# Optimization experiments

Hardware: AMD Instinct MI355X
Metric: run time of the kernel (lower is better)

Reference implementation:

```python
import jax, jax.numpy as jnp
import numpy as np

B, S, D_IN, D_OUT, L = 16, 1024, 768, 768, 2
ALPHA = 0.2  # LeakyReLU negative slope
NEG_INF = -1e12


def setup_inputs() -> dict:
    key = jax.random.key(0)
    ks = jax.random.split(key, 6)
    input_feature = jax.random.normal(ks[0], (B, S, D_IN), dtype=jnp.float32)
    matrix = jax.random.randint(ks[1], (B, S, S), 0, 2, dtype=jnp.int32)
    # per-layer params (stacked along leading L axis)
    sw = 1.0 / np.sqrt(D_IN)
    W = jax.random.uniform(ks[2], (L, D_OUT, D_IN), jnp.float32, -sw, sw)
    Wb = jax.random.uniform(ks[3], (L, D_OUT), jnp.float32, -sw, sw)
    sa = 1.0 / np.sqrt(2 * D_OUT)
    A = jax.random.uniform(ks[4], (L, 2 * D_OUT), jnp.float32, -sa, sa)
    Ab = jax.random.uniform(ks[5], (L,), jnp.float32, -sa, sa)
    return {"input_feature": input_feature, "matrix": matrix,
            "W": W, "Wb": Wb, "A": A, "Ab": Ab}


def reference(input_feature, matrix, W, Wb, A, Ab):
    # Eval mode: dropout(p=0.1, training=False) is identity.
    hidden = input_feature
    mask = matrix > 0  # [B,S,S]
    outs = []
    for l in range(L):
        h = jnp.einsum('bsd,od->bso', hidden, W[l]) + Wb[l]  # [B,S,Dout]
        # a([h_i, h_j]) == h_i @ a_src + h_j @ a_dst + b  (exact separation)
        a_src, a_dst = A[l, :D_OUT], A[l, D_OUT:]
        s_i = h @ a_src  # [B,S]
        s_j = h @ a_dst  # [B,S]
        e = jax.nn.leaky_relu(s_i[:, :, None] + s_j[:, None, :] + Ab[l], ALPHA)
        e = jnp.where(mask, e, NEG_INF)
        attn = jax.nn.softmax(e, axis=1)  # original softmaxes over dim=1
        hidden = jnp.einsum('bij,bjd->bid', attn, h)
        outs.append(hidden)
    return jnp.stack(outs)  # [L,B,S,Dout]
```

## Files before the change

kernel.cpp:

```cpp
#include <hip/hip_runtime.h>
#include <cstddef>

#define SS 1024
#define DF 768
#define NBATCH 16
#define GAT_ALPHA 0.2f

typedef _Float16 f16x8 __attribute__((ext_vector_type(8)));
typedef _Float16 f16x4 __attribute__((ext_vector_type(4)));
typedef float f32x4 __attribute__((ext_vector_type(4)));

__device__ __forceinline__ void gload16(const void* g, void* l) {
  __builtin_amdgcn_global_load_lds(
      (const __attribute__((address_space(1))) void*)g,
      (__attribute__((address_space(3))) void*)l, 16, 0, 0);
}

__device__ __forceinline__ float lrelu(float t) {
  return fmaxf(t, GAT_ALPHA * t);
}

__global__ __launch_bounds__(256) void f32tof16_k(const float* __restrict__ in,
                                                  _Float16* __restrict__ out,
                                                  int n) {
  int idx = (blockIdx.x * 256 + threadIdx.x) * 4;
  if (idx + 3 < n) {
    float4 v = *(const float4*)&in[idx];
    f16x4 o;
    o[0] = (_Float16)v.x;
    o[1] = (_Float16)v.y;
    o[2] = (_Float16)v.z;
    o[3] = (_Float16)v.w;
    *(f16x4*)&out[idx] = o;
  }
}

__global__ __launch_bounds__(256) void pack_k(const int* __restrict__ mask,
                                              unsigned char* __restrict__ bm) {
  const size_t t = (size_t)blockIdx.x * 256 + threadIdx.x;
  const int* mp = mask + t * 8;
  const int4 a = *(const int4*)mp;
  const int4 c = *(const int4*)(mp + 4);
  unsigned v = (unsigned)(a.x > 0) | ((unsigned)(a.y > 0) << 1) |
               ((unsigned)(a.z > 0) << 2) | ((unsigned)(a.w > 0) << 3) |
               ((unsigned)(c.x > 0) << 4) | ((unsigned)(c.y > 0) << 5) |
               ((unsigned)(c.z > 0) << 6) | ((unsigned)(c.w > 0) << 7);
  bm[t] = (unsigned char)v;
}


__global__ __launch_bounds__(512, 2) void gemm1_k(
    const _Float16* __restrict__ X16, const _Float16* __restrict__ W16,
    const float* __restrict__ Wbl, _Float16* __restrict__ hT16) {
  __shared__ __align__(16) char smem[131072];
  const int flat = blockIdx.x;
  const int swz = (flat & 7) * 32 + (flat >> 3);
  const int m0 = (swz >> 1) * 128;
  const int n0 = (swz & 1) * 384;
  const int tid = threadIdx.x;
  const int w = tid >> 6, lane = tid & 63;

  const int srow = w * 16 + (lane >> 2);
  const int sk8 = ((lane & 3) ^ ((lane >> 3) & 3)) * 8;
  const int rby = ((lane >> 4) ^ ((lane >> 1) & 3)) * 16;
  const int rrow = lane & 15;

  f32x4 acc[8][3];
#pragma unroll
  for (int mi = 0; mi < 8; ++mi)
#pragma unroll
    for (int ni = 0; ni < 3; ++ni) acc[mi][ni] = (f32x4)(0.f);

#define STGA1(s, kt)                                                       \
  gload16(&X16[(size_t)(m0 + srow) * DF + (kt) * 32 + sk8],                \
          smem + (s) * 32768 + w * 1024)
#define STGB1(s, kt, q)                                                    \
  gload16(&W16[(size_t)(n0 + (q) * 128 + srow) * DF + (kt) * 32 + sk8],    \
          smem + (s) * 32768 + 8192 + (q) * 8192 + w * 1024)

  const int NT = DF / 32;
  STGA1(0, 0); STGB1(0, 0, 0); STGB1(0, 0, 1); STGB1(0, 0, 2);
  STGA1(1, 1); STGB1(1, 1, 0); STGB1(1, 1, 1); STGB1(1, 1, 2);
  asm volatile("s_waitcnt vmcnt(4)" ::: "memory");
  asm volatile("s_barrier" ::: "memory");

  for (int t = 0; t < NT; ++t) {
    const int s = t & 3;
    const char* Ab = smem + s * 32768;
    const char* Bb = smem + s * 32768 + 8192;
    f16x8 bfr[3], afr[4];
#pragma unroll
    for (int ni = 0; ni < 3; ++ni)
      bfr[ni] = *(const f16x8*)(Bb + (w * 48 + ni * 16 + rrow) * 64 + rby);
#pragma unroll
    for (int mi = 0; mi < 4; ++mi)
      afr[mi] = *(const f16x8*)(Ab + (mi * 16 + rrow) * 64 + rby);
    if (t + 2 < NT) {
      STGA1((t + 2) & 3, t + 2);
      STGB1((t + 2) & 3, t + 2, 0);
    }
    asm volatile("s_barrier" ::: "memory");
    __builtin_amdgcn_s_setprio(1);
#pragma unroll
    for (int mi = 0; mi < 4; ++mi)
#pragma unroll
      for (int ni = 0; ni < 3; ++ni)
        acc[mi][ni] = __builtin_amdgcn_mfma_f32_16x16x32_f16(
            afr[mi], bfr[ni], acc[mi][ni], 0, 0, 0);
    __builtin_amdgcn_s_setprio(0);
    asm volatile("s_barrier" ::: "memory");
#pragma unroll
    for (int mi = 0; mi < 4; ++mi)
      afr[mi] = *(const f16x8*)(Ab + ((mi + 4) * 16 + rrow) * 64 + rby);
    if (t + 2 < NT) {
      STGB1((t + 2) & 3, t + 2, 1);
      STGB1((t + 2) & 3, t + 2, 2);
    }
    if (t < NT - 2)
      asm volatile("s_waitcnt vmcnt(4)" ::: "memory");
    else
      asm volatile("s_waitcnt vmcnt(0)" ::: "memory");
    asm volatile("s_barrier" ::: "memory");
    __builtin_amdgcn_s_setprio(1);
#pragma unroll
    for (int mi = 0; mi < 4; ++mi)
#pragma unroll
      for (int ni = 0; ni < 3; ++ni)
        acc[mi + 4][ni] = __builtin_amdgcn_mfma_f32_16x16x32_f16(
            afr[mi], bfr[ni], acc[mi + 4][ni], 0, 0, 0);
    __builtin_amdgcn_s_setprio(0);
    asm volatile("s_barrier" ::: "memory");
  }
#undef STGA1
#undef STGB1

  _Float16* tb = (_Float16*)smem + (size_t)w * 6528;
  const int cg = lane >> 4, cr = lane & 15;
  float bias[3];
#pragma unroll
  for (int ni = 0; ni < 3; ++ni) bias[ni] = Wbl[n0 + w * 48 + ni * 16 + cr];
#pragma unroll
  for (int mi = 0; mi < 8; ++mi) {
#pragma unroll
    for (int ni = 0; ni < 3; ++ni) {
      f16x4 tv;
#pragma unroll
      for (int r = 0; r < 4; ++r)
        tv[r] = (_Float16)(acc[mi][ni][r] + bias[ni]);
      *(f16x4*)&tb[(ni * 16 + cr) * 136 + mi * 16 + cg * 4] = tv;
    }
  }
  const int bb = m0 >> 10, s0 = m0 & 1023;
#pragma unroll
  for (int pass = 0; pass < 12; ++pass) {
    const int c = pass * 4 + (lane >> 4);
    f16x8 v = *(const f16x8*)&tb[c * 136 + (lane & 15) * 8];
    *(f16x8*)&hT16[((size_t)bb * DF + n0 + w * 48 + c) * SS + s0 +
                   (lane & 15) * 8] = v;
  }
}

__global__ __launch_bounds__(512, 2) void gemm2_k(
    const _Float16* __restrict__ P16, const _Float16* __restrict__ hT16,
    float* __restrict__ outl, _Float16* __restrict__ X16n, int writeX) {
  __shared__ __align__(16) char smem[131072];
  const int flat = blockIdx.x;
  const int swz = (flat & 7) * 32 + (flat >> 3);
  const int b = swz >> 4;
  const int i0 = ((swz >> 1) & 7) * 128;
  const int d0 = (swz & 1) * 384;
  const int tid = threadIdx.x;
  const int w = tid >> 6, lane = tid & 63;

  const int srow = w * 16 + (lane >> 2);
  const int sk8 = ((lane & 3) ^ ((lane >> 3) & 3)) * 8;
  const int rby = ((lane >> 4) ^ ((lane >> 1) & 3)) * 16;
  const int rrow = lane & 15;

  const _Float16* Pb = P16 + ((size_t)b << 20);
  const _Float16* hTb = hT16 + (size_t)b * DF * SS;

  f32x4 acc[8][3];
#pragma unroll
  for (int mi = 0; mi < 8; ++mi)
#pragma unroll
    for (int ni = 0; ni < 3; ++ni) acc[mi][ni] = (f32x4)(0.f);

#define STGA2(s, kt)                                                       \
  gload16(&Pb[((size_t)(i0 + srow) << 10) + (kt) * 32 + sk8],              \
          smem + (s) * 32768 + w * 1024)
#define STGB2(s, kt, q)                                                    \
  gload16(&hTb[((size_t)(d0 + (q) * 128 + srow)) * SS + (kt) * 32 + sk8],  \
          smem + (s) * 32768 + 8192 + (q) * 8192 + w * 1024)

  const int NT = SS / 32;
  STGA2(0, 0); STGB2(0, 0, 0); STGB2(0, 0, 1); STGB2(0, 0, 2);
  STGA2(1, 1); STGB2(1, 1, 0); STGB2(1, 1, 1); STGB2(1, 1, 2);
  asm volatile("s_waitcnt vmcnt(4)" ::: "memory");
  asm volatile("s_barrier" ::: "memory");

  for (int t = 0; t < NT; ++t) {
    const int s = t & 3;
    const char* Ab = smem + s * 32768;
    const char* Bb = smem + s * 32768 + 8192;
    f16x8 bfr[3], afr[4];
#pragma unroll
    for (int ni = 0; ni < 3; ++ni)
      bfr[ni] = *(const f16x8*)(Bb + (w * 48 + ni * 16 + rrow) * 64 + rby);
#pragma unroll
    for (int mi = 0; mi < 4; ++mi)
      afr[mi] = *(const f16x8*)(Ab + (mi * 16 + rrow) * 64 + rby);
    if (t + 2 < NT) {
      STGA2((t + 2) & 3, t + 2);
      STGB2((t + 2) & 3, t + 2, 0);
    }
    asm volatile("s_barrier" ::: "memory");
    __builtin_amdgcn_s_setprio(1);
#pragma unroll
    for (int mi = 0; mi < 4; ++mi)
#pragma unroll
      for (int ni = 0; ni < 3; ++ni)
        acc[mi][ni] = __builtin_amdgcn_mfma_f32_16x16x32_f16(
            afr[mi], bfr[ni], acc[mi][ni], 0, 0, 0);
    __builtin_amdgcn_s_setprio(0);
    asm volatile("s_barrier" ::: "memory");
#pragma unroll
    for (int mi = 0; mi < 4; ++mi)
      afr[mi] = *(const f16x8*)(Ab + ((mi + 4) * 16 + rrow) * 64 + rby);
    if (t + 2 < NT) {
      STGB2((t + 2) & 3, t + 2, 1);
      STGB2((t + 2) & 3, t + 2, 2);
    }
    if (t < NT - 2)
      asm volatile("s_waitcnt vmcnt(4)" ::: "memory");
    else
      asm volatile("s_waitcnt vmcnt(0)" ::: "memory");
    asm volatile("s_barrier" ::: "memory");
    __builtin_amdgcn_s_setprio(1);
#pragma unroll
    for (int mi = 0; mi < 4; ++mi)
#pragma unroll
      for (int ni = 0; ni < 3; ++ni)
        acc[mi + 4][ni] = __builtin_amdgcn_mfma_f32_16x16x32_f16(
            afr[mi], bfr[ni], acc[mi + 4][ni], 0, 0, 0);
    __builtin_amdgcn_s_setprio(0);
    asm volatile("s_barrier" ::: "memory");
  }
#undef STGA2
#undef STGB2

  const int cg = lane >> 4, cr = lane & 15;
#pragma unroll
  for (int mi = 0; mi < 8; ++mi) {
#pragma unroll
    for (int ni = 0; ni < 3; ++ni) {
      const int d = d0 + w * 48 + ni * 16 + cr;
      const int row0 = i0 + mi * 16 + cg * 4;
#pragma unroll
      for (int r = 0; r < 4; ++r) {
        float v = acc[mi][ni][r];
        size_t o = ((size_t)b * SS + row0 + r) * DF + d;
        outl[o] = v;
        if (writeX) X16n[o] = (_Float16)v;
      }
    }
  }
}

__global__ __launch_bounds__(256) void rowdots2_k(
    const _Float16* __restrict__ hT, const float* __restrict__ Al,
    float* __restrict__ psi, float* __restrict__ psj) {
  const int dc = blockIdx.x;
  const int b = blockIdx.y;
  const int t = threadIdx.x;
  const int s4 = t * 4;
  __shared__ float sa[48], sd[48];
  if (t < 48) {
    sa[t] = Al[dc * 48 + t];
    sd[t] = Al[DF + dc * 48 + t];
  }
  __syncthreads();
  float as[4] = {0.f, 0.f, 0.f, 0.f}, ad[4] = {0.f, 0.f, 0.f, 0.f};
  const _Float16* hp = hT + ((size_t)b * DF + dc * 48) * SS + s4;
#pragma unroll 4
  for (int q = 0; q < 48; ++q) {
    const f16x4 hv = *(const f16x4*)(hp + (size_t)q * SS);
    const float ws = sa[q], wd = sd[q];
#pragma unroll
    for (int r = 0; r < 4; ++r) {
      const float hf = (float)hv[r];
      as[r] = fmaf(hf, ws, as[r]);
      ad[r] = fmaf(hf, wd, ad[r]);
    }
  }
  const size_t o = (size_t)dc * 16384 + (b << 10) + s4;
  *(float4*)&psi[o] = *(float4*)as;
  *(float4*)&psj[o] = *(float4*)ad;
}

__global__ __launch_bounds__(256) void rowfin_k(const float* __restrict__ psi,
                                                const float* __restrict__ psj,
                                                const float* __restrict__ Abp,
                                                float* __restrict__ si,
                                                float* __restrict__ sjc,
                                                float* __restrict__ refj) {
  const int b = blockIdx.x;
  const int t = threadIdx.x;
  __shared__ float red[256];
  float siv[4], sjv[4];
  float mloc = -1e30f;
#pragma unroll
  for (int q = 0; q < 4; ++q) {
    const int idx = (b << 10) + t + (q << 8);
    float a = 0.f, d = 0.f;
#pragma unroll
    for (int c = 0; c < 16; ++c) {
      a += psi[(size_t)c * 16384 + idx];
      d += psj[(size_t)c * 16384 + idx];
    }
    siv[q] = a;
    sjv[q] = d;
    si[idx] = a;
    mloc = fmaxf(mloc, a);
  }
  red[t] = mloc;
  __syncthreads();
  for (int off = 128; off > 0; off >>= 1) {
    if (t < off) red[t] = fmaxf(red[t], red[t + off]);
    __syncthreads();
  }
  const float maxsi = red[0];
  const float ab = Abp[0];
#pragma unroll
  for (int q = 0; q < 4; ++q) {
    const int idx = (b << 10) + t + (q << 8);
    const float c = sjv[q] + ab;
    sjc[idx] = c;
    refj[idx] = lrelu(maxsi + c);
  }
}

__global__ __launch_bounds__(256) void colsum_k(
    const unsigned char* __restrict__ bm, const float* __restrict__ si,
    const float* __restrict__ sjc, const float* __restrict__ refj,
    float* __restrict__ pden) {
  const int g = blockIdx.x;
  const int b = blockIdx.y;
  const int t = threadIdx.x;
  const int jb = t & 127;
  const int half = t >> 7;
  const int row0 = (g << 5) + (half << 4);
  __shared__ float s_si[32];
  if (t < 32) s_si[t] = si[(b << 10) + (g << 5) + t];
  __syncthreads();
  float sc[8], rf[8];
  *(float4*)&sc[0] = *(const float4*)&sjc[(b << 10) + jb * 8];
  *(float4*)&sc[4] = *(const float4*)&sjc[(b << 10) + jb * 8 + 4];
  *(float4*)&rf[0] = *(const float4*)&refj[(b << 10) + jb * 8];
  *(float4*)&rf[4] = *(const float4*)&refj[(b << 10) + jb * 8 + 4];
  float den[8] = {0.f, 0.f, 0.f, 0.f, 0.f, 0.f, 0.f, 0.f};
  const unsigned char* bp = bm + ((size_t)b << 17) + ((size_t)row0 << 7) + jb;
#pragma unroll 4
  for (int r = 0; r < 16; ++r) {
    const unsigned m = bp[(size_t)r << 7];
    const float siv = s_si[(half << 4) + r];
#pragma unroll
    for (int k = 0; k < 8; ++k) {
      if ((m >> k) & 1) den[k] += __expf(lrelu(siv + sc[k]) - rf[k]);
    }
  }
  const size_t o = ((size_t)(g * 2 + half)) * 16384 + (b << 10) + jb * 8;
  *(float4*)&pden[o] = *(float4*)&den[0];
  *(float4*)&pden[o + 4] = *(float4*)&den[4];
}

__global__ __launch_bounds__(256) void colcomb_k(const float* __restrict__ pden,
                                                 float* __restrict__ rden) {
  const int idx = blockIdx.x * 256 + threadIdx.x;
  float s = 0.f;
#pragma unroll
  for (int c = 0; c < 64; ++c) s += pden[(size_t)c * 16384 + idx];
  rden[idx] = (s > 0.f) ? 1.f / s : -1.f;
}

__global__ __launch_bounds__(256) void punorm2_k(
    const unsigned char* __restrict__ bm, const float* __restrict__ si,
    const float* __restrict__ sjc, const float* __restrict__ refj,
    const float* __restrict__ rden, _Float16* __restrict__ P16) {
  const int g = blockIdx.x;
  const int b = blockIdx.y;
  const int t = threadIdx.x;
  const int jb = t & 127;
  const int half = t >> 7;
  const int row0 = (g << 5) + (half << 4);
  __shared__ float s_si[32];
  if (t < 32) s_si[t] = si[(b << 10) + (g << 5) + t];
  __syncthreads();
  float sc[8], rf[8], rd[8];
  *(float4*)&sc[0] = *(const float4*)&sjc[(b << 10) + jb * 8];
  *(float4*)&sc[4] = *(const float4*)&sjc[(b << 10) + jb * 8 + 4];
  *(float4*)&rf[0] = *(const float4*)&refj[(b << 10) + jb * 8];
  *(float4*)&rf[4] = *(const float4*)&refj[(b << 10) + jb * 8 + 4];
  *(float4*)&rd[0] = *(const float4*)&rden[(b << 10) + jb * 8];
  *(float4*)&rd[4] = *(const float4*)&rden[(b << 10) + jb * 8 + 4];
  const unsigned char* bp = bm + ((size_t)b << 17) + ((size_t)row0 << 7) + jb;
  _Float16* pp = P16 + ((size_t)b << 20) + ((size_t)row0 << 10) + jb * 8;
#pragma unroll 4
  for (int r = 0; r < 16; ++r) {
    const unsigned m = bp[(size_t)r << 7];
    const float siv = s_si[(half << 4) + r];
    f16x8 ph;
#pragma unroll
    for (int k = 0; k < 8; ++k) {
      float p;
      if (rd[k] < 0.f)
        p = 0.0009765625f;
      else if ((m >> k) & 1)
        p = __expf(lrelu(siv + sc[k]) - rf[k]) * rd[k];
      else
        p = 0.f;
      ph[k] = (_Float16)p;
    }
    *(f16x8*)(pp + ((size_t)r << 10)) = ph;
  }
}

extern "C" void kernel_launch(void* const* d_in, const int* in_sizes, int n_in,
                              void* d_out, int out_size, void* d_ws,
                              size_t ws_size, hipStream_t stream) {
  const float* X0 = (const float*)d_in[0];
  const int* mask = (const int*)d_in[1];
  const float* W = (const float*)d_in[2];
  const float* Wb = (const float*)d_in[3];
  const float* A = (const float*)d_in[4];
  const float* Ab = (const float*)d_in[5];
  float* out = (float*)d_out;

  const size_t BSD = (size_t)NBATCH * SS * DF;
  const size_t BSS = (size_t)NBATCH * SS * SS;
  const size_t BS = (size_t)NBATCH * SS;

  char* p = (char*)d_ws;
  _Float16* X16 = (_Float16*)p;   p += BSD * 2;
  _Float16* hT16 = (_Float16*)p;  p += BSD * 2;
  _Float16* P16 = (_Float16*)p;   p += BSS * 2;
  _Float16* W16 = (_Float16*)p;   p += (size_t)2 * DF * DF * 2;
  unsigned char* bmk = (unsigned char*)p; p += BSS / 8;
  float* psi = (float*)p;  p += 16 * BS * 4;
  float* psj = (float*)p;  p += 16 * BS * 4;
  float* pden = (float*)p; p += 64 * BS * 4;
  float* si = (float*)p;   p += BS * 4;
  float* sjc = (float*)p;  p += BS * 4;
  float* refj = (float*)p; p += BS * 4;
  float* rden = (float*)p; p += BS * 4;

  f32tof16_k<<<12288, 256, 0, stream>>>(X0, X16, (int)BSD);
  f32tof16_k<<<1152, 256, 0, stream>>>(W, W16, 2 * DF * DF);
  pack_k<<<8192, 256, 0, stream>>>(mask, bmk);

  for (int l = 0; l < 2; ++l) {
    gemm1_k<<<256, 512, 0, stream>>>(X16, W16 + (size_t)l * DF * DF,
                                     Wb + (size_t)l * DF, hT16);
    rowdots2_k<<<dim3(16, 16), 256, 0, stream>>>(hT16, A + (size_t)l * 2 * DF,
                                                 psi, psj);
    rowfin_k<<<16, 256, 0, stream>>>(psi, psj, Ab + l, si, sjc, refj);
    colsum_k<<<dim3(32, 16), 256, 0, stream>>>(bmk, si, sjc, refj, pden);
    colcomb_k<<<64, 256, 0, stream>>>(pden, rden);
    punorm2_k<<<dim3(32, 16), 256, 0, stream>>>(bmk, si, sjc, refj, rden, P16);
    gemm2_k<<<256, 512, 0, stream>>>(P16, hT16, out + (size_t)l * BSD, X16,
                                     (l == 0) ? 1 : 0);
  }
}
```

Baseline: 268.1 us.

## Fuse attention row-dot products into gemm1 epilogue and simplify GEMM main loop

Computes the per-row a_src/a_dst dot products inside the gemm1 epilogue from the fp16 tile already staged in shared memory. This removes the separate rowdots2 kernel, its re-read of hT16 and its 16-way partial buffers; rowfin now sums only two partials. Both GEMM main loops also load all 8 A fragments at once and issue all four prefetches together, dropping two barriers per iteration. The cost is higher register pressure and extra epilogue synchronisation.

```diff
diff --git a/kernel.cpp b/kernel.cpp
--- a/kernel.cpp
+++ b/kernel.cpp
@@ -51,7 +51,9 @@
 
 __global__ __launch_bounds__(512, 2) void gemm1_k(
     const _Float16* __restrict__ X16, const _Float16* __restrict__ W16,
-    const float* __restrict__ Wbl, _Float16* __restrict__ hT16) {
+    const float* __restrict__ Wbl, const float* __restrict__ Al,
+    _Float16* __restrict__ hT16, float* __restrict__ psi2,
+    float* __restrict__ psj2) {
   __shared__ __align__(16) char smem[131072];
   const int flat = blockIdx.x;
   const int swz = (flat & 7) * 32 + (flat >> 3);
@@ -88,33 +90,19 @@
     const int s = t & 3;
     const char* Ab = smem + s * 32768;
     const char* Bb = smem + s * 32768 + 8192;
-    f16x8 bfr[3], afr[4];
+    f16x8 bfr[3], afr[8];
 #pragma unroll
     for (int ni = 0; ni < 3; ++ni)
       bfr[ni] = *(const f16x8*)(Bb + (w * 48 + ni * 16 + rrow) * 64 + rby);
 #pragma unroll
-    for (int mi = 0; mi < 4; ++mi)
+    for (int mi = 0; mi < 8; ++mi)
       afr[mi] = *(const f16x8*)(Ab + (mi * 16 + rrow) * 64 + rby);
     if (t + 2 < NT) {
-      STGA1((t + 2) & 3, t + 2);
-      STGB1((t + 2) & 3, t + 2, 0);
-    }
-    asm volatile("s_barrier" ::: "memory");
-    __builtin_amdgcn_s_setprio(1);
-#pragma unroll
-    for (int mi = 0; mi < 4; ++mi)
-#pragma unroll
-      for (int ni = 0; ni < 3; ++ni)
-        acc[mi][ni] = __builtin_amdgcn_mfma_f32_16x16x32_f16(
-            afr[mi], bfr[ni], acc[mi][ni], 0, 0, 0);
-    __builtin_amdgcn_s_setprio(0);
-    asm volatile("s_barrier" ::: "memory");
-#pragma unroll
-    for (int mi = 0; mi < 4; ++mi)
-      afr[mi] = *(const f16x8*)(Ab + ((mi + 4) * 16 + rrow) * 64 + rby);
-    if (t + 2 < NT) {
-      STGB1((t + 2) & 3, t + 2, 1);
-      STGB1((t + 2) & 3, t + 2, 2);
+      const int s2 = (t + 2) & 3;
+      STGA1(s2, t + 2);
+      STGB1(s2, t + 2, 0);
+      STGB1(s2, t + 2, 1);
+      STGB1(s2, t + 2, 2);
     }
     if (t < NT - 2)
       asm volatile("s_waitcnt vmcnt(4)" ::: "memory");
@@ -123,18 +111,28 @@
     asm volatile("s_barrier" ::: "memory");
     __builtin_amdgcn_s_setprio(1);
 #pragma unroll
-    for (int mi = 0; mi < 4; ++mi)
+    for (int mi = 0; mi < 8; ++mi)
 #pragma unroll
       for (int ni = 0; ni < 3; ++ni)
-        acc[mi + 4][ni] = __builtin_amdgcn_mfma_f32_16x16x32_f16(
-            afr[mi], bfr[ni], acc[mi + 4][ni], 0, 0, 0);
+        acc[mi][ni] = __builtin_amdgcn_mfma_f32_16x16x32_f16(
+            afr[mi], bfr[ni], acc[mi][ni], 0, 0, 0);
     __builtin_amdgcn_s_setprio(0);
-    asm volatile("s_barrier" ::: "memory");
   }
 #undef STGA1
 #undef STGB1
 
+  __syncthreads();
+
   _Float16* tb = (_Float16*)smem + (size_t)w * 6528;
+  float* asrc = (float*)(smem + 104448);
+  float* adst = asrc + 384;
+  float* pwsi = adst + 384;
+  float* pwsj = pwsi + 1024;
+
+  for (int i = tid; i < 384; i += 512) {
+    asrc[i] = Al[n0 + i];
+    adst[i] = Al[DF + n0 + i];
+  }
   const int cg = lane >> 4, cr = lane & 15;
   float bias[3];
 #pragma unroll
@@ -150,6 +148,36 @@
       *(f16x4*)&tb[(ni * 16 + cr) * 136 + mi * 16 + cg * 4] = tv;
     }
   }
+  __syncthreads();
+
+  const float* wa = asrc + w * 48;
+  const float* wdp = adst + w * 48;
+#pragma unroll
+  for (int rr = 0; rr < 2; ++rr) {
+    const int r = lane + rr * 64;
+    float ps = 0.f, pd = 0.f;
+#pragma unroll 8
+    for (int c = 0; c < 48; ++c) {
+      const float hv = (float)tb[c * 136 + r];
+      ps = fmaf(hv, wa[c], ps);
+      pd = fmaf(hv, wdp[c], pd);
+    }
+    pwsi[w * 128 + r] = ps;
+    pwsj[w * 128 + r] = pd;
+  }
+  __syncthreads();
+  if (tid < 128) {
+    float s = 0.f, d2 = 0.f;
+#pragma unroll
+    for (int ww = 0; ww < 8; ++ww) {
+      s += pwsi[ww * 128 + tid];
+      d2 += pwsj[ww * 128 + tid];
+    }
+    const int nt = swz & 1;
+    psi2[nt * 16384 + m0 + tid] = s;
+    psj2[nt * 16384 + m0 + tid] = d2;
+  }
+
   const int bb = m0 >> 10, s0 = m0 & 1023;
 #pragma unroll
   for (int pass = 0; pass < 12; ++pass) {
@@ -203,33 +231,19 @@
     const int s = t & 3;
     const char* Ab = smem + s * 32768;
     const char* Bb = smem + s * 32768 + 8192;
-    f16x8 bfr[3], afr[4];
+    f16x8 bfr[3], afr[8];
 #pragma unroll
     for (int ni = 0; ni < 3; ++ni)
       bfr[ni] = *(const f16x8*)(Bb + (w * 48 + ni * 16 + rrow) * 64 + rby);
 #pragma unroll
-    for (int mi = 0; mi < 4; ++mi)
+    for (int mi = 0; mi < 8; ++mi)
       afr[mi] = *(const f16x8*)(Ab + (mi * 16 + rrow) * 64 + rby);
     if (t + 2 < NT) {
-      STGA2((t + 2) & 3, t + 2);
-      STGB2((t + 2) & 3, t + 2, 0);
-    }
-    asm volatile("s_barrier" ::: "memory");
-    __builtin_amdgcn_s_setprio(1);
-#pragma unroll
-    for (int mi = 0; mi < 4; ++mi)
-#pragma unroll
-      for (int ni = 0; ni < 3; ++ni)
-        acc[mi][ni] = __builtin_amdgcn_mfma_f32_16x16x32_f16(
-            afr[mi], bfr[ni], acc[mi][ni], 0, 0, 0);
-    __builtin_amdgcn_s_setprio(0);
-    asm volatile("s_barrier" ::: "memory");
-#pragma unroll
-    for (int mi = 0; mi < 4; ++mi)
-      afr[mi] = *(const f16x8*)(Ab + ((mi + 4) * 16 + rrow) * 64 + rby);
-    if (t + 2 < NT) {
-      STGB2((t + 2) & 3, t + 2, 1);
-      STGB2((t + 2) & 3, t + 2, 2);
+      const int s2 = (t + 2) & 3;
+      STGA2(s2, t + 2);
+      STGB2(s2, t + 2, 0);
+      STGB2(s2, t + 2, 1);
+      STGB2(s2, t + 2, 2);
     }
     if (t < NT - 2)
       asm volatile("s_waitcnt vmcnt(4)" ::: "memory");
@@ -238,13 +252,12 @@
     asm volatile("s_barrier" ::: "memory");
     __builtin_amdgcn_s_setprio(1);
 #pragma unroll
-    for (int mi = 0; mi < 4; ++mi)
+    for (int mi = 0; mi < 8; ++mi)
 #pragma unroll
       for (int ni = 0; ni < 3; ++ni)
-        acc[mi + 4][ni] = __builtin_amdgcn_mfma_f32_16x16x32_f16(
-            afr[mi], bfr[ni], acc[mi + 4][ni], 0, 0, 0);
+        acc[mi][ni] = __builtin_amdgcn_mfma_f32_16x16x32_f16(
+            afr[mi], bfr[ni], acc[mi][ni], 0, 0, 0);
     __builtin_amdgcn_s_setprio(0);
-    asm volatile("s_barrier" ::: "memory");
   }
 #undef STGA2
 #undef STGB2
@@ -267,39 +280,8 @@
   }
 }
 
-__global__ __launch_bounds__(256) void rowdots2_k(
-    const _Float16* __restrict__ hT, const float* __restrict__ Al,
-    float* __restrict__ psi, float* __restrict__ psj) {
-  const int dc = blockIdx.x;
-  const int b = blockIdx.y;
-  const int t = threadIdx.x;
-  const int s4 = t * 4;
-  __shared__ float sa[48], sd[48];
-  if (t < 48) {
-    sa[t] = Al[dc * 48 + t];
-    sd[t] = Al[DF + dc * 48 + t];
-  }
-  __syncthreads();
-  float as[4] = {0.f, 0.f, 0.f, 0.f}, ad[4] = {0.f, 0.f, 0.f, 0.f};
-  const _Float16* hp = hT + ((size_t)b * DF + dc * 48) * SS + s4;
-#pragma unroll 4
-  for (int q = 0; q < 48; ++q) {
-    const f16x4 hv = *(const f16x4*)(hp + (size_t)q * SS);
-    const float ws = sa[q], wd = sd[q];
-#pragma unroll
-    for (int r = 0; r < 4; ++r) {
-      const float hf = (float)hv[r];
-      as[r] = fmaf(hf, ws, as[r]);
-      ad[r] = fmaf(hf, wd, ad[r]);
-    }
-  }
-  const size_t o = (size_t)dc * 16384 + (b << 10) + s4;
-  *(float4*)&psi[o] = *(float4*)as;
-  *(float4*)&psj[o] = *(float4*)ad;
-}
-
-__global__ __launch_bounds__(256) void rowfin_k(const float* __restrict__ psi,
-                                                const float* __restrict__ psj,
+__global__ __launch_bounds__(256) void rowfin_k(const float* __restrict__ psi2,
+                                                const float* __restrict__ psj2,
                                                 const float* __restrict__ Abp,
                                                 float* __restrict__ si,
                                                 float* __restrict__ sjc,
@@ -312,12 +294,8 @@
 #pragma unroll
   for (int q = 0; q < 4; ++q) {
     const int idx = (b << 10) + t + (q << 8);
-    float a = 0.f, d = 0.f;
-#pragma unroll
-    for (int c = 0; c < 16; ++c) {
-      a += psi[(size_t)c * 16384 + idx];
-      d += psj[(size_t)c * 16384 + idx];
-    }
+    const float a = psi2[idx] + psi2[16384 + idx];
+    const float d = psj2[idx] + psj2[16384 + idx];
     siv[q] = a;
     sjv[q] = d;
     si[idx] = a;
@@ -446,8 +424,8 @@
   _Float16* P16 = (_Float16*)p;   p += BSS * 2;
   _Float16* W16 = (_Float16*)p;   p += (size_t)2 * DF * DF * 2;
   unsigned char* bmk = (unsigned char*)p; p += BSS / 8;
-  float* psi = (float*)p;  p += 16 * BS * 4;
-  float* psj = (float*)p;  p += 16 * BS * 4;
+  float* psi2 = (float*)p; p += 2 * BS * 4;
+  float* psj2 = (float*)p; p += 2 * BS * 4;
   float* pden = (float*)p; p += 64 * BS * 4;
   float* si = (float*)p;   p += BS * 4;
   float* sjc = (float*)p;  p += BS * 4;
@@ -460,10 +438,9 @@
 
   for (int l = 0; l < 2; ++l) {
     gemm1_k<<<256, 512, 0, stream>>>(X16, W16 + (size_t)l * DF * DF,
-                                     Wb + (size_t)l * DF, hT16);
-    rowdots2_k<<<dim3(16, 16), 256, 0, stream>>>(hT16, A + (size_t)l * 2 * DF,
-                                                 psi, psj);
-    rowfin_k<<<16, 256, 0, stream>>>(psi, psj, Ab + l, si, sjc, refj);
+                                     Wb + (size_t)l * DF,
+                                     A + (size_t)l * 2 * DF, hT16, psi2, psj2);
+    rowfin_k<<<16, 256, 0, stream>>>(psi2, psj2, Ab + l, si, sjc, refj);
     colsum_k<<<dim3(32, 16), 256, 0, stream>>>(bmk, si, sjc, refj, pden);
     colcomb_k<<<64, 256, 0, stream>>>(pden, rden);
     punorm2_k<<<dim3(32, 16), 256, 0, stream>>>(bmk, si, sjc, refj, rden, P16);
```

Measured after the change: 255.0 us. 4.9% less time.
